# Performance work log

Measured on AMD Instinct MI355X. Metric: run time of the kernel, lower is better.

The kernel has to match this reference:

```python
import jax, jax.numpy as jnp
import numpy as np

B, N0, N, CP, CS, C1, C2 = 8, 8192, 2048, 512, 256, 256, 256
BN_EPS = 1e-3
SLOPE = 0.01


def setup_inputs() -> dict:
    key = jax.random.key(0)
    ks = jax.random.split(key, 10)
    xyz = jax.random.normal(ks[0], (B, 3, N0), jnp.float32)
    skip = jax.random.normal(ks[1], (B, CS, N0), jnp.float32)
    xyz_prev = jax.random.normal(ks[2], (B, 3, N), jnp.float32)
    feat_prev = jax.random.normal(ks[3], (B, CP, N), jnp.float32)
    W1 = jax.random.normal(ks[4], (C1, CP + CS), jnp.float32) * 0.05
    g1 = jax.random.uniform(ks[5], (C1,), jnp.float32, 0.5, 1.5)
    b1 = jax.random.normal(ks[6], (C1,), jnp.float32) * 0.1
    W2 = jax.random.normal(ks[7], (C2, C1), jnp.float32) * 0.05
    g2 = jax.random.uniform(ks[8], (C2,), jnp.float32, 0.5, 1.5)
    b2 = jax.random.normal(ks[9], (C2,), jnp.float32) * 0.1
    return dict(xyz=xyz, skip=skip, xyz_prev=xyz_prev, feat_prev=feat_prev,
                W1=W1, g1=g1, b1=b1, W2=W2, g2=g2, b2=b2)


def _three_interp(xyz, xyz_prev, feat_prev):
    # xyz: [B,3,N0] query points; xyz_prev: [B,3,N] source; feat_prev: [B,CP,N]
    x = xyz.transpose(0, 2, 1)        # [B,N0,3]
    y = xyz_prev.transpose(0, 2, 1)   # [B,N,3]
    d2 = ((x * x).sum(-1)[:, :, None] + (y * y).sum(-1)[:, None, :]
          - 2.0 * jnp.einsum('bnd,bmd->bnm', x, y))   # [B,N0,N] squared dists
    neg_vals, idx = jax.lax.top_k(-d2, 3)             # 3 smallest distances
    d2nn = jnp.maximum(-neg_vals, 1e-10)              # dist*dist with clamp
    inv = 1.0 / (d2nn + 1e-8)
    w = inv / inv.sum(-1, keepdims=True)              # [B,N0,3]
    # gather feat_prev[b,c,idx[b,n,k]] -> [B,CP,N0,3]
    gathered = jnp.take_along_axis(feat_prev[:, :, None, :], idx[:, None, :, :], axis=3)
    return (gathered * w[:, None, :, :]).sum(-1)      # [B,CP,N0]


def _conv_bn_lrelu(x, W, g, b):
    # conv1x1 (no bias) + BatchNorm1d (training-mode batch stats, eps=1e-3) + LeakyReLU(0.01)
    y = jnp.einsum('oc,bcn->bon', W, x)
    mean = y.mean(axis=(0, 2), keepdims=True)
    var = ((y - mean) ** 2).mean(axis=(0, 2), keepdims=True)
    y = (y - mean) * jax.lax.rsqrt(var + BN_EPS) * g[None, :, None] + b[None, :, None]
    return jnp.where(y >= 0, y, SLOPE * y)


def reference(xyz, skip, xyz_prev, feat_prev, W1, g1, b1, W2, g2, b2):
    nf = _three_interp(xyz, xyz_prev, feat_prev)      # [B,CP,N0]
    nf = jnp.concatenate([nf, skip], axis=1)          # [B,CP+CS,N0]
    nf = _conv_bn_lrelu(nf, W1, g1, b1)
    nf = _conv_bn_lrelu(nf, W2, g2, b2)
    return xyz, nf
```

## Files before the change

### kernel.cpp

```cpp
#include <hip/hip_runtime.h>
#include <hip/hip_bf16.h>

using bf16 = __hip_bfloat16;

constexpr int B  = 8;
constexpr int N0 = 8192;
constexpr int NS = 2048;
constexpr int CP = 512;
constexpr int CS = 256;
constexpr int C1 = 256;
constexpr int C2 = 256;
constexpr int K1 = CP + CS;
constexpr int COLS = B * N0;
constexpr float BN_EPS = 1e-3f;
constexpr float SLOPE  = 0.01f;

typedef short  short8 __attribute__((ext_vector_type(8)));
typedef float  f32x4  __attribute__((ext_vector_type(4)));

typedef __attribute__((address_space(1))) unsigned int gas_uint;
typedef __attribute__((address_space(3))) unsigned int las_uint;

__device__ __forceinline__ unsigned short f2bu(float f) {
  unsigned int u = __float_as_uint(f);
  return (unsigned short)((u + 0x7fffu + ((u >> 16) & 1u)) >> 16);
}
__device__ __forceinline__ float bu2f(unsigned short v) {
  return __uint_as_float((unsigned int)v << 16);
}

__global__ __launch_bounds__(256) void prep_kernel(
    const float* __restrict__ W1, const float* __restrict__ W2,
    unsigned short* __restrict__ W1b, unsigned short* __restrict__ W2b,
    float* __restrict__ stats)
{
  int id = blockIdx.x * 256 + threadIdx.x;
  if (id < 1024) stats[id] = 0.0f;
  if (id < C1 * K1) W1b[id] = f2bu(W1[id]);
  if (id < C2 * C1) W2b[id] = f2bu(W2[id]);
}

__global__ __launch_bounds__(256) void knn_kernel(
    const float* __restrict__ xyz, const float* __restrict__ xyz_prev,
    float* __restrict__ wq, int* __restrict__ iq)
{
#pragma clang fp contract(off)
  __shared__ float4 sp[NS];
  __shared__ float  md[4][64][3];
  __shared__ int    mi[4][64][3];
  const int b = blockIdx.y;
  const float* xp = xyz_prev + (size_t)b * 3 * NS;
  for (int j = threadIdx.x; j < NS; j += 256) {
    float x = xp[j], y = xp[NS + j], z = xp[2 * NS + j];
    sp[j] = make_float4(x, y, z, (x * x + y * y) + z * z);
  }
  __syncthreads();

  const int q  = threadIdx.x & 63;
  const int sl = threadIdx.x >> 6;
  const int n  = blockIdx.x * 64 + q;
  const float* xq = xyz + (size_t)b * 3 * N0;
  float qx = xq[n], qy = xq[N0 + n], qz = xq[2 * N0 + n];
  float qq = (qx * qx + qy * qy) + qz * qz;

  float d0 = 1e30f, d1 = 1e30f, d2 = 1e30f;
  int   i0 = 0, i1 = 0, i2 = 0;
  const int j0 = sl * (NS / 4), j1 = j0 + (NS / 4);
#pragma unroll 4
  for (int j = j0; j < j1; ++j) {
    float4 p = sp[j];
    float dot = (qx * p.x + qy * p.y) + qz * p.z;
    float d = (qq + p.w) - 2.0f * dot;
    if (d < d0)      { d2 = d1; i2 = i1; d1 = d0; i1 = i0; d0 = d; i0 = j; }
    else if (d < d1) { d2 = d1; i2 = i1; d1 = d;  i1 = j; }
    else if (d < d2) { d2 = d;  i2 = j; }
  }
  md[sl][q][0] = d0; md[sl][q][1] = d1; md[sl][q][2] = d2;
  mi[sl][q][0] = i0; mi[sl][q][1] = i1; mi[sl][q][2] = i2;
  __syncthreads();

  if (threadIdx.x < 64) {
    float e0 = 1e30f, e1 = 1e30f, e2 = 1e30f;
    int   k0 = 0, k1 = 0, k2 = 0;
#pragma unroll
    for (int s = 0; s < 4; ++s) {
#pragma unroll
      for (int t = 0; t < 3; ++t) {
        float d = md[s][q][t]; int ii = mi[s][q][t];
        if (d < e0)      { e2 = e1; k2 = k1; e1 = e0; k1 = k0; e0 = d; k0 = ii; }
        else if (d < e1) { e2 = e1; k2 = k1; e1 = d;  k1 = ii; }
        else if (d < e2) { e2 = d;  k2 = ii; }
      }
    }
    e0 = fmaxf(e0, 1e-10f); e1 = fmaxf(e1, 1e-10f); e2 = fmaxf(e2, 1e-10f);
    float v0 = 1.0f / (e0 + 1e-8f), v1 = 1.0f / (e1 + 1e-8f), v2 = 1.0f / (e2 + 1e-8f);
    float s = (v0 + v1) + v2;
    const int gi = (b * N0 + n) * 3;
    wq[gi + 0] = v0 / s; wq[gi + 1] = v1 / s; wq[gi + 2] = v2 / s;
    iq[gi + 0] = k0;     iq[gi + 1] = k1;     iq[gi + 2] = k2;
  }
}

__global__ __launch_bounds__(256) void interp_kernel(
    const float* __restrict__ feat_prev, const int* __restrict__ iq,
    const float* __restrict__ wq, unsigned short* __restrict__ Xt)
{
  __shared__ unsigned short sf[16 * 2048];
  const int bx = blockIdx.x;
  const int b  = bx >> 6;
  const int cg = (bx >> 1) & 31;
  const int nh = bx & 1;
  const int c0 = cg * 16;
  const float* fp = feat_prev + ((size_t)b * CP + c0) * NS;

  for (int id = threadIdx.x; id < 8192; id += 256) {
    float4 v = reinterpret_cast<const float4*>(fp)[id];
    ushort4 o;
    o.x = f2bu(v.x); o.y = f2bu(v.y); o.z = f2bu(v.z); o.w = f2bu(v.w);
    *reinterpret_cast<ushort4*>(&sf[id * 4]) = o;
  }
  __syncthreads();

  const int nbase = nh * 4096;
  for (int it = 0; it < 16; ++it) {
    const int n    = nbase + it * 256 + threadIdx.x;
    const int gcol = b * N0 + n;
    const int gq   = gcol * 3;
    const int i0 = iq[gq], i1 = iq[gq + 1], i2 = iq[gq + 2];
    const float w0 = wq[gq], w1 = wq[gq + 1], w2 = wq[gq + 2];
    unsigned short outv[16];
#pragma unroll
    for (int c = 0; c < 16; ++c) {
      const unsigned short* row = &sf[c * 2048];
      float v = w0 * bu2f(row[i0]) + w1 * bu2f(row[i1]) + w2 * bu2f(row[i2]);
      outv[c] = f2bu(v);
    }
    unsigned short* dst = Xt + (size_t)gcol * K1 + c0;
    *reinterpret_cast<short8*>(dst)     = *reinterpret_cast<short8*>(&outv[0]);
    *reinterpret_cast<short8*>(dst + 8) = *reinterpret_cast<short8*>(&outv[8]);
  }
}

__global__ __launch_bounds__(256) void skipt_kernel(
    const float* __restrict__ skip, unsigned short* __restrict__ Xt)
{
  __shared__ float T[64][65];
  const int kt   = blockIdx.x & 3;
  const int ct   = blockIdx.x >> 2;
  const int col0 = ct * 64;
  const int b    = col0 >> 13;
  const int n0   = col0 & 8191;
  const float* src = skip + ((size_t)b * CS + kt * 64) * N0 + n0;

  for (int id = threadIdx.x; id < 1024; id += 256) {
    int r = id >> 4, q = id & 15;
    float4 v = *reinterpret_cast<const float4*>(src + (size_t)r * N0 + q * 4);
    T[r][q * 4 + 0] = v.x; T[r][q * 4 + 1] = v.y;
    T[r][q * 4 + 2] = v.z; T[r][q * 4 + 3] = v.w;
  }
  __syncthreads();
  for (int id = threadIdx.x; id < 512; id += 256) {
    int n = id >> 3, q = id & 7;
    alignas(16) unsigned short tmp[8];
#pragma unroll
    for (int j = 0; j < 8; ++j) tmp[j] = f2bu(T[q * 8 + j][n]);
    *reinterpret_cast<short8*>(Xt + (size_t)(col0 + n) * K1 + CP + kt * 64 + q * 8) =
        *reinterpret_cast<short8*>(tmp);
  }
}

__global__ __launch_bounds__(256, 2) void gemm1_kernel(
    const unsigned short* __restrict__ W1b, const unsigned short* __restrict__ Xt,
    unsigned short* __restrict__ Y1t, float* __restrict__ stats)
{
  __shared__ unsigned short Bs[2 * 128 * 64];

  const int tid   = threadIdx.x;
  const int gcol0 = blockIdx.x * 128;

  const int wv = tid >> 6, lane = tid & 63;
  const int wm = wv * 64;
  const int qm = lane & 15, quad = lane >> 4;
  const int lr = lane >> 3, lc = lane & 7;
  const int sw_src = (lc ^ lr) * 8;
  const int sw_rd  = qm & 7;

  f32x4 acc[4][8];
#pragma unroll
  for (int i = 0; i < 4; ++i)
#pragma unroll
    for (int j = 0; j < 8; ++j) acc[i][j] = (f32x4){0.f, 0.f, 0.f, 0.f};

  auto stageB = [&](int kt, int buf) {
    const int kof = kt * 64 + sw_src;
#pragma unroll
    for (int t = 0; t < 4; ++t) {
      const int ch = wv * 4 + t;
      const int r  = ch * 8 + lr;
      __builtin_amdgcn_global_load_lds(
          (const gas_uint*)(Xt + (size_t)(gcol0 + r) * K1 + kof),
          (las_uint*)(&Bs[buf * (128 * 64) + ch * 512]), 16, 0, 0);
    }
  };
  auto loadA = [&](int kt, short8 (&af)[2][4]) {
#pragma unroll
    for (int h = 0; h < 2; ++h)
#pragma unroll
      for (int i = 0; i < 4; ++i)
        af[h][i] = *reinterpret_cast<const short8*>(
            W1b + (size_t)(wm + i * 16 + qm) * K1 + kt * 64 + h * 32 + quad * 8);
  };
  auto compute = [&](const short8 (&af)[2][4], int buf) {
    const unsigned short* Bb = &Bs[buf * (128 * 64)];
#pragma unroll
    for (int h = 0; h < 2; ++h) {
      short8 bf[8];
#pragma unroll
      for (int j = 0; j < 8; ++j)
        bf[j] = *reinterpret_cast<const short8*>(
            &Bb[(j * 16 + qm) * 64 + ((h * 4 + quad) ^ sw_rd) * 8]);
#pragma unroll
      for (int i = 0; i < 4; ++i)
#pragma unroll
        for (int j = 0; j < 8; ++j)
          acc[i][j] = __builtin_amdgcn_mfma_f32_16x16x32_bf16(af[h][i], bf[j], acc[i][j], 0, 0, 0);
    }
  };

  short8 afA[2][4], afB[2][4];
  loadA(0, afA);
  stageB(0, 0);
  __syncthreads();

  for (int kt = 0; kt < K1 / 64; kt += 2) {
    stageB(kt + 1, 1);
    loadA(kt + 1, afB);
    compute(afA, 0);
    __syncthreads();
    if (kt + 2 < K1 / 64) { stageB(kt + 2, 0); loadA(kt + 2, afA); }
    compute(afB, 1);
    if (kt + 2 < K1 / 64) __syncthreads();
  }

#pragma unroll
  for (int i = 0; i < 4; ++i) {
    const int mb = wm + i * 16 + quad * 4;
    float s[4] = {0.f, 0.f, 0.f, 0.f}, s2[4] = {0.f, 0.f, 0.f, 0.f};
#pragma unroll
    for (int j = 0; j < 8; ++j) {
      const int gc = gcol0 + j * 16 + qm;
      ushort4 o;
      o.x = f2bu(acc[i][j][0]); o.y = f2bu(acc[i][j][1]);
      o.z = f2bu(acc[i][j][2]); o.w = f2bu(acc[i][j][3]);
      *reinterpret_cast<ushort4*>(Y1t + (size_t)gc * C1 + mb) = o;
#pragma unroll
      for (int r = 0; r < 4; ++r) {
        float v = acc[i][j][r];
        s[r] += v; s2[r] += v * v;
      }
    }
#pragma unroll
    for (int m = 1; m < 16; m <<= 1) {
#pragma unroll
      for (int r = 0; r < 4; ++r) { s[r] += __shfl_xor(s[r], m); s2[r] += __shfl_xor(s2[r], m); }
    }
    if (qm == 0) {
#pragma unroll
      for (int r = 0; r < 4; ++r) {
        atomicAdd(&stats[mb + r], s[r]);
        atomicAdd(&stats[C1 + mb + r], s2[r]);
      }
    }
  }
}

__global__ __launch_bounds__(256) void affine_kernel(
    const float* __restrict__ s, const float* __restrict__ g,
    const float* __restrict__ bb, float* __restrict__ a)
{
  int c = threadIdx.x;
  float inv = 1.0f / (float)COLS;
  float mean = s[c] * inv;
  float var  = s[C1 + c] * inv - mean * mean;
  float sc   = g[c] / sqrtf(var + BN_EPS);
  a[c]      = sc;
  a[C1 + c] = bb[c] - mean * sc;
}

__global__ __launch_bounds__(256, 2) void gemm2_kernel(
    const unsigned short* __restrict__ W2b, const unsigned short* __restrict__ Y1t,
    const float* __restrict__ aff, float* __restrict__ out_nf,
    float* __restrict__ stats2)
{
  __shared__ unsigned short Bs[2][128][72];

  const int tid   = threadIdx.x;
  const int gcol0 = blockIdx.x * 128;
  const int b     = gcol0 >> 13;
  const int ncol0 = gcol0 & 8191;

  const int wv = tid >> 6, lane = tid & 63;
  const int wm = wv * 64;
  const int qm = lane & 15, quad = lane >> 4;
  const int sn = tid >> 1;
  const int sck = (tid & 1) * 4;

  f32x4 acc[4][8];
#pragma unroll
  for (int i = 0; i < 4; ++i)
#pragma unroll
    for (int j = 0; j < 8; ++j) acc[i][j] = (f32x4){0.f, 0.f, 0.f, 0.f};

  short8 af[2][4];
  short8 breg[4];
  auto loadA = [&](int kt) {
#pragma unroll
    for (int h = 0; h < 2; ++h)
#pragma unroll
      for (int i = 0; i < 4; ++i)
        af[h][i] = *reinterpret_cast<const short8*>(
            W2b + (size_t)(wm + i * 16 + qm) * C1 + kt * 64 + h * 32 + quad * 8);
  };
  auto loadB = [&](int kt) {
#pragma unroll
    for (int t = 0; t < 4; ++t)
      breg[t] = *reinterpret_cast<const short8*>(
          Y1t + (size_t)(gcol0 + sn) * C1 + kt * 64 + (sck + t) * 8);
  };
  auto xformWrite = [&](int kt, int buf) {
#pragma unroll
    for (int t = 0; t < 4; ++t) {
      const int c0 = kt * 64 + (sck + t) * 8;
      float4 sc0 = *reinterpret_cast<const float4*>(aff + c0);
      float4 sc1 = *reinterpret_cast<const float4*>(aff + c0 + 4);
      float4 sh0 = *reinterpret_cast<const float4*>(aff + C1 + c0);
      float4 sh1 = *reinterpret_cast<const float4*>(aff + C1 + c0 + 4);
      alignas(16) unsigned short tmp[8];
#pragma unroll
      for (int j = 0; j < 4; ++j) {
        float v = bu2f((unsigned short)breg[t][j]) * (&sc0.x)[j] + (&sh0.x)[j];
        v = (v >= 0.f) ? v : SLOPE * v;
        tmp[j] = f2bu(v);
      }
#pragma unroll
      for (int j = 0; j < 4; ++j) {
        float v = bu2f((unsigned short)breg[t][4 + j]) * (&sc1.x)[j] + (&sh1.x)[j];
        v = (v >= 0.f) ? v : SLOPE * v;
        tmp[4 + j] = f2bu(v);
      }
      *reinterpret_cast<short8*>(&Bs[buf][sn][(sck + t) * 8]) =
          *reinterpret_cast<short8*>(tmp);
    }
  };
  auto compute = [&](int buf) {
#pragma unroll
    for (int h = 0; h < 2; ++h) {
      short8 bf[8];
#pragma unroll
      for (int j = 0; j < 8; ++j)
        bf[j] = *reinterpret_cast<const short8*>(
            &Bs[buf][j * 16 + qm][(h * 4 + quad) * 8]);
#pragma unroll
      for (int i = 0; i < 4; ++i)
#pragma unroll
        for (int j = 0; j < 8; ++j)
          acc[i][j] = __builtin_amdgcn_mfma_f32_16x16x32_bf16(af[h][i], bf[j], acc[i][j], 0, 0, 0);
    }
  };

  loadB(0);
  xformWrite(0, 0);
  __syncthreads();

  for (int kt = 0; kt < C1 / 64; ++kt) {
    loadA(kt);
    if (kt + 1 < C1 / 64) loadB(kt + 1);
    compute(kt & 1);
    if (kt + 1 < C1 / 64) {
      xformWrite(kt + 1, (kt + 1) & 1);
      __syncthreads();
    }
  }

#pragma unroll
  for (int i = 0; i < 4; ++i) {
    const int mb = wm + i * 16 + quad * 4;
    float s[4] = {0.f, 0.f, 0.f, 0.f}, s2[4] = {0.f, 0.f, 0.f, 0.f};
#pragma unroll
    for (int j = 0; j < 8; ++j) {
      const int col = ncol0 + j * 16 + qm;
#pragma unroll
      for (int r = 0; r < 4; ++r) {
        float v = acc[i][j][r];
        out_nf[((size_t)b * C2 + mb + r) * N0 + col] = v;
        s[r] += v; s2[r] += v * v;
      }
    }
#pragma unroll
    for (int m = 1; m < 16; m <<= 1) {
#pragma unroll
      for (int r = 0; r < 4; ++r) { s[r] += __shfl_xor(s[r], m); s2[r] += __shfl_xor(s2[r], m); }
    }
    if (qm == 0) {
#pragma unroll
      for (int r = 0; r < 4; ++r) {
        atomicAdd(&stats2[mb + r], s[r]);
        atomicAdd(&stats2[C2 + mb + r], s2[r]);
      }
    }
  }
}

__global__ __launch_bounds__(256) void finalize_kernel(float* __restrict__ nf,
                                                       const float* __restrict__ aff)
{
  int id4 = blockIdx.x * 256 + threadIdx.x;
  int e = id4 * 4;
  int c = (e % (C2 * N0)) / N0;
  float sc = aff[c], sh = aff[C1 + c];
  float4 v = reinterpret_cast<float4*>(nf)[id4];
  v.x = v.x * sc + sh; v.x = (v.x >= 0.f) ? v.x : SLOPE * v.x;
  v.y = v.y * sc + sh; v.y = (v.y >= 0.f) ? v.y : SLOPE * v.y;
  v.z = v.z * sc + sh; v.z = (v.z >= 0.f) ? v.z : SLOPE * v.z;
  v.w = v.w * sc + sh; v.w = (v.w >= 0.f) ? v.w : SLOPE * v.w;
  reinterpret_cast<float4*>(nf)[id4] = v;
}

__global__ __launch_bounds__(256) void copy_xyz_kernel(const float* __restrict__ xyz,
                                                       float* __restrict__ out)
{
  int id = blockIdx.x * 256 + threadIdx.x;
  reinterpret_cast<float4*>(out)[id] = reinterpret_cast<const float4*>(xyz)[id];
}

extern "C" void kernel_launch(void* const* d_in, const int* in_sizes, int n_in,
                              void* d_out, int out_size, void* d_ws, size_t ws_size,
                              hipStream_t stream)
{
  const float* xyz       = (const float*)d_in[0];
  const float* skip      = (const float*)d_in[1];
  const float* xyz_prev  = (const float*)d_in[2];
  const float* feat_prev = (const float*)d_in[3];
  const float* W1        = (const float*)d_in[4];
  const float* g1        = (const float*)d_in[5];
  const float* b1        = (const float*)d_in[6];
  const float* W2        = (const float*)d_in[7];
  const float* g2        = (const float*)d_in[8];
  const float* b2        = (const float*)d_in[9];

  float* out    = (float*)d_out;
  float* out_nf = out + (size_t)B * 3 * N0;

  char* ws = (char*)d_ws;
  float*          wq    = (float*)(ws + 0);
  int*            iq    = (int*)  (ws + 786432);
  unsigned short* W1b   = (unsigned short*)(ws + 1572864);
  unsigned short* W2b   = (unsigned short*)(ws + 1966080);
  float*          stats = (float*)(ws + 2097152);
  float*          aff   = (float*)(ws + 2101248);
  unsigned short* Y1t   = (unsigned short*)(ws + 2105344);
  unsigned short* Xt    = (unsigned short*)(ws + 35659776);

  prep_kernel<<<768, 256, 0, stream>>>(W1, W2, W1b, W2b, stats);
  knn_kernel<<<dim3(N0 / 64, B), 256, 0, stream>>>(xyz, xyz_prev, wq, iq);
  interp_kernel<<<512, 256, 0, stream>>>(feat_prev, iq, wq, Xt);
  skipt_kernel<<<4096, 256, 0, stream>>>(skip, Xt);
  gemm1_kernel<<<COLS / 128, 256, 0, stream>>>(W1b, Xt, Y1t, stats);
  affine_kernel<<<1, 256, 0, stream>>>(stats, g1, b1, aff);
  gemm2_kernel<<<COLS / 128, 256, 0, stream>>>(W2b, Y1t, aff, out_nf, stats + 512);
  affine_kernel<<<1, 256, 0, stream>>>(stats + 512, g2, b2, aff + 512);
  finalize_kernel<<<(C2 * N0 * B) / (4 * 256), 256, 0, stream>>>(out_nf, aff + 512);
  copy_xyz_kernel<<<(B * 3 * N0) / (4 * 256), 256, 0, stream>>>(xyz, out);
}
```

Before: 477.6 us.

## Deepen GEMM load pipelines, stage Y1 stores via LDS, split kNN scan chains

The kNN scan now keeps two independent top-3 candidate chains per thread, which breaks the serial compare dependency, and merges them at the end. gemm1 keeps two K-tiles in flight using explicit vmcnt waits and raw barriers instead of __syncthreads. It also writes its bf16 output through an LDS scratch tile so the global stores are full 16-byte coalesced rows. gemm2 is fully unrolled with double-buffered A and B register prefetch. The gains come from hiding memory latency and coalescing stores, at the cost of extra LDS, more registers, and hand-tuned wait counts that are fragile.

After: 494.3 us. 1.03x slower.

```diff
diff --git a/kernel.cpp b/kernel.cpp
--- a/kernel.cpp
+++ b/kernel.cpp
@@ -21,6 +21,11 @@
 typedef __attribute__((address_space(1))) unsigned int gas_uint;
 typedef __attribute__((address_space(3))) unsigned int las_uint;
 
+#define BARX() do { asm volatile("" ::: "memory"); __builtin_amdgcn_s_barrier(); asm volatile("" ::: "memory"); } while (0)
+#define VM12()  asm volatile("s_waitcnt vmcnt(12)" ::: "memory")
+#define VM0()   asm volatile("s_waitcnt vmcnt(0)"  ::: "memory")
+#define LGKM0() asm volatile("s_waitcnt lgkmcnt(0)" ::: "memory")
+
 __device__ __forceinline__ unsigned short f2bu(float f) {
   unsigned int u = __float_as_uint(f);
   return (unsigned short)((u + 0x7fffu + ((u >> 16) & 1u)) >> 16);
@@ -63,20 +68,39 @@
   float qx = xq[n], qy = xq[N0 + n], qz = xq[2 * N0 + n];
   float qq = (qx * qx + qy * qy) + qz * qz;
 
-  float d0 = 1e30f, d1 = 1e30f, d2 = 1e30f;
-  int   i0 = 0, i1 = 0, i2 = 0;
-  const int j0 = sl * (NS / 4), j1 = j0 + (NS / 4);
-#pragma unroll 4
-  for (int j = j0; j < j1; ++j) {
-    float4 p = sp[j];
-    float dot = (qx * p.x + qy * p.y) + qz * p.z;
-    float d = (qq + p.w) - 2.0f * dot;
-    if (d < d0)      { d2 = d1; i2 = i1; d1 = d0; i1 = i0; d0 = d; i0 = j; }
-    else if (d < d1) { d2 = d1; i2 = i1; d1 = d;  i1 = j; }
-    else if (d < d2) { d2 = d;  i2 = j; }
-  }
-  md[sl][q][0] = d0; md[sl][q][1] = d1; md[sl][q][2] = d2;
-  mi[sl][q][0] = i0; mi[sl][q][1] = i1; mi[sl][q][2] = i2;
+  const int j0 = sl * (NS / 4);
+  float a0 = 1e30f, a1 = 1e30f, a2 = 1e30f;
+  int   ai0 = 0, ai1 = 0, ai2 = 0;
+  float c0 = 1e30f, c1 = 1e30f, c2 = 1e30f;
+  int   ci0 = 0, ci1 = 0, ci2 = 0;
+#pragma unroll 2
+  for (int jj = 0; jj < NS / 8; ++jj) {
+    const int ja = j0 + jj, jc = j0 + NS / 8 + jj;
+    float4 pa = sp[ja];
+    float4 pc = sp[jc];
+    float dota = (qx * pa.x + qy * pa.y) + qz * pa.z;
+    float da = (qq + pa.w) - 2.0f * dota;
+    float dotc = (qx * pc.x + qy * pc.y) + qz * pc.z;
+    float dc = (qq + pc.w) - 2.0f * dotc;
+    if (da < a0)      { a2 = a1; ai2 = ai1; a1 = a0; ai1 = ai0; a0 = da; ai0 = ja; }
+    else if (da < a1) { a2 = a1; ai2 = ai1; a1 = da; ai1 = ja; }
+    else if (da < a2) { a2 = da; ai2 = ja; }
+    if (dc < c0)      { c2 = c1; ci2 = ci1; c1 = c0; ci1 = ci0; c0 = dc; ci0 = jc; }
+    else if (dc < c1) { c2 = c1; ci2 = ci1; c1 = dc; ci1 = jc; }
+    else if (dc < c2) { c2 = dc; ci2 = jc; }
+  }
+  {
+    float dv[3] = {c0, c1, c2}; int iv[3] = {ci0, ci1, ci2};
+#pragma unroll
+    for (int t = 0; t < 3; ++t) {
+      float d = dv[t]; int ii = iv[t];
+      if (d < a0)      { a2 = a1; ai2 = ai1; a1 = a0; ai1 = ai0; a0 = d; ai0 = ii; }
+      else if (d < a1) { a2 = a1; ai2 = ai1; a1 = d;  ai1 = ii; }
+      else if (d < a2) { a2 = d;  ai2 = ii; }
+    }
+  }
+  md[sl][q][0] = a0; md[sl][q][1] = a1; md[sl][q][2] = a2;
+  mi[sl][q][0] = ai0; mi[sl][q][1] = ai1; mi[sl][q][2] = ai2;
   __syncthreads();
 
   if (threadIdx.x < 64) {
@@ -173,7 +197,8 @@
     const unsigned short* __restrict__ W1b, const unsigned short* __restrict__ Xt,
     unsigned short* __restrict__ Y1t, float* __restrict__ stats)
 {
-  __shared__ unsigned short Bs[2 * 128 * 64];
+  __shared__ unsigned short Bs[2][128 * 64];
+  __shared__ unsigned short scr[64][264];
 
   const int tid   = threadIdx.x;
   const int gcol0 = blockIdx.x * 128;
@@ -199,7 +224,7 @@
       const int r  = ch * 8 + lr;
       __builtin_amdgcn_global_load_lds(
           (const gas_uint*)(Xt + (size_t)(gcol0 + r) * K1 + kof),
-          (las_uint*)(&Bs[buf * (128 * 64) + ch * 512]), 16, 0, 0);
+          (las_uint*)(&Bs[buf][ch * 512]), 16, 0, 0);
     }
   };
   auto loadA = [&](int kt, short8 (&af)[2][4]) {
@@ -211,7 +236,7 @@
             W1b + (size_t)(wm + i * 16 + qm) * K1 + kt * 64 + h * 32 + quad * 8);
   };
   auto compute = [&](const short8 (&af)[2][4], int buf) {
-    const unsigned short* Bb = &Bs[buf * (128 * 64)];
+    const unsigned short* Bb = &Bs[buf][0];
 #pragma unroll
     for (int h = 0; h < 2; ++h) {
       short8 bf[8];
@@ -228,18 +253,20 @@
   };
 
   short8 afA[2][4], afB[2][4];
-  loadA(0, afA);
-  stageB(0, 0);
-  __syncthreads();
+  stageB(0, 0); loadA(0, afA);
+  stageB(1, 1); loadA(1, afB);
 
   for (int kt = 0; kt < K1 / 64; kt += 2) {
-    stageB(kt + 1, 1);
-    loadA(kt + 1, afB);
+    VM12();
+    BARX();
     compute(afA, 0);
-    __syncthreads();
+    BARX();
     if (kt + 2 < K1 / 64) { stageB(kt + 2, 0); loadA(kt + 2, afA); }
+    if (kt < 10) { VM12(); } else { VM0(); }
+    BARX();
     compute(afB, 1);
-    if (kt + 2 < K1 / 64) __syncthreads();
+    BARX();
+    if (kt + 3 < K1 / 64) { stageB(kt + 3, 1); loadA(kt + 3, afB); }
   }
 
 #pragma unroll
@@ -248,11 +275,6 @@
     float s[4] = {0.f, 0.f, 0.f, 0.f}, s2[4] = {0.f, 0.f, 0.f, 0.f};
 #pragma unroll
     for (int j = 0; j < 8; ++j) {
-      const int gc = gcol0 + j * 16 + qm;
-      ushort4 o;
-      o.x = f2bu(acc[i][j][0]); o.y = f2bu(acc[i][j][1]);
-      o.z = f2bu(acc[i][j][2]); o.w = f2bu(acc[i][j][3]);
-      *reinterpret_cast<ushort4*>(Y1t + (size_t)gc * C1 + mb) = o;
 #pragma unroll
       for (int r = 0; r < 4; ++r) {
         float v = acc[i][j][r];
@@ -271,6 +293,32 @@
         atomicAdd(&stats[C1 + mb + r], s2[r]);
       }
     }
+  }
+
+#pragma unroll
+  for (int half = 0; half < 2; ++half) {
+#pragma unroll
+    for (int i = 0; i < 4; ++i) {
+      const int mb = wm + i * 16 + quad * 4;
+#pragma unroll
+      for (int jj = 0; jj < 4; ++jj) {
+        const int j = half * 4 + jj;
+        ushort4 o;
+        o.x = f2bu(acc[i][j][0]); o.y = f2bu(acc[i][j][1]);
+        o.z = f2bu(acc[i][j][2]); o.w = f2bu(acc[i][j][3]);
+        *reinterpret_cast<ushort4*>(&scr[jj * 16 + qm][mb]) = o;
+      }
+    }
+    LGKM0();
+    BARX();
+#pragma unroll
+    for (int u = 0; u < 8; ++u) {
+      const int flat = tid * 16 + u * 4096;
+      const int r = flat >> 9, c = (flat & 511) >> 1;
+      short8 v = *reinterpret_cast<const short8*>(&scr[r][c]);
+      *reinterpret_cast<short8*>(Y1t + (((size_t)(gcol0 + half * 64 + r)) << 8) + c) = v;
+    }
+    if (half == 0) BARX();
   }
 }
 
@@ -311,9 +359,10 @@
 #pragma unroll
     for (int j = 0; j < 8; ++j) acc[i][j] = (f32x4){0.f, 0.f, 0.f, 0.f};
 
-  short8 af[2][4];
-  short8 breg[4];
-  auto loadA = [&](int kt) {
+  short8 afA[2][4], afB[2][4];
+  short8 bregA[4], bregB[4];
+
+  auto loadA = [&](int kt, short8 (&af)[2][4]) {
 #pragma unroll
     for (int h = 0; h < 2; ++h)
 #pragma unroll
@@ -321,13 +370,13 @@
         af[h][i] = *reinterpret_cast<const short8*>(
             W2b + (size_t)(wm + i * 16 + qm) * C1 + kt * 64 + h * 32 + quad * 8);
   };
-  auto loadB = [&](int kt) {
+  auto loadB = [&](int kt, short8 (&breg)[4]) {
 #pragma unroll
     for (int t = 0; t < 4; ++t)
       breg[t] = *reinterpret_cast<const short8*>(
           Y1t + (size_t)(gcol0 + sn) * C1 + kt * 64 + (sck + t) * 8);
   };
-  auto xformWrite = [&](int kt, int buf) {
+  auto xformWrite = [&](const short8 (&breg)[4], int kt, int buf) {
 #pragma unroll
     for (int t = 0; t < 4; ++t) {
       const int c0 = kt * 64 + (sck + t) * 8;
@@ -352,7 +401,7 @@
           *reinterpret_cast<short8*>(tmp);
     }
   };
-  auto compute = [&](int buf) {
+  auto compute = [&](const short8 (&af)[2][4], int buf) {
 #pragma unroll
     for (int h = 0; h < 2; ++h) {
       short8 bf[8];
@@ -368,19 +417,22 @@
     }
   };
 
-  loadB(0);
-  xformWrite(0, 0);
-  __syncthreads();
-
-  for (int kt = 0; kt < C1 / 64; ++kt) {
-    loadA(kt);
-    if (kt + 1 < C1 / 64) loadB(kt + 1);
-    compute(kt & 1);
-    if (kt + 1 < C1 / 64) {
-      xformWrite(kt + 1, (kt + 1) & 1);
-      __syncthreads();
-    }
-  }
+  loadB(0, bregA); loadA(0, afA);
+  loadB(1, bregB); loadA(1, afB);
+  xformWrite(bregA, 0, 0);
+  LGKM0(); BARX();
+  compute(afA, 0);
+  xformWrite(bregB, 1, 1);
+  loadB(2, bregA); loadA(2, afA);
+  LGKM0(); BARX();
+  compute(afB, 1);
+  xformWrite(bregA, 2, 0);
+  loadB(3, bregB); loadA(3, afB);
+  LGKM0(); BARX();
+  compute(afA, 0);
+  xformWrite(bregB, 3, 1);
+  LGKM0(); BARX();
+  compute(afB, 1);
 
 #pragma unroll
   for (int i = 0; i < 4; ++i) {
```
